# Performance work log

Hardware: AMD Instinct MI355X
Metric: run time of the kernel (lower is better)

## Reference

```python
import jax, jax.numpy as jnp
from jax import lax
import numpy as np

N = 64  # nPoints
N_ANGS = N * (N - 1) // 2

# lexicographic (top, btm) pair order used by OrthonormalMatrixGenerationSystem
_tops, _btms = np.triu_indices(N, k=1)
TOPS = jnp.asarray(_tops, dtype=jnp.int32)
BTMS = jnp.asarray(_btms, dtype=jnp.int32)


def build_R(angles, mus):
    """Sequential Givens-rotation chain: R = diag(mus) @ G_{nAngs-1} ... G_0 @ I."""
    def step(R, inp):
        ang, t, b = inp
        c, s = jnp.cos(ang), jnp.sin(ang)
        rt, rb = R[t], R[b]
        R = R.at[t].set(c * rt - s * rb).at[b].set(s * rt + c * rb)
        return R, None

    R0 = jnp.eye(N, dtype=angles.dtype)
    R, _ = lax.scan(step, R0, (angles, TOPS, BTMS))
    return mus[:, None] * R


def setup_inputs() -> dict:
    key = jax.random.key(0)
    k1, k2 = jax.random.split(key)
    X = jax.random.normal(k1, (N, 300000), dtype=jnp.float32)
    angles = jax.random.normal(k2, (N_ANGS,), dtype=jnp.float32)
    mus = jnp.ones((N,), dtype=jnp.float32)
    return {"X": X, "angles": angles, "mus": mus}


def reference(X, angles, mus):
    # mode='Analysis': Y = R @ X
    R = build_R(angles, mus)
    return R @ X
```

## Files before the change

### kernel.cpp

```cpp
#include <hip/hip_runtime.h>


#define NPTS  64
#define NANG  2016
#define NCOLS 300000
#define NC4   (NCOLS / 4)

typedef float v4 __attribute__((ext_vector_type(4)));

#define PSTR 68


__device__ __forceinline__ float rl(float x, int lane) {
    return __uint_as_float(__builtin_amdgcn_readlane(__float_as_uint(x), lane));
}

template<int T, int TB, int TA, int NG>
__device__ __forceinline__ void groups_run(float (&S)[NPTS],
                                           const float (&c)[NG], const float (&s)[NG],
                                           float* __restrict__ slab, int lane)
{
    if constexpr (T < TB) {
        constexpr int g   = T - TA;
        constexpr int LEN = 63 - T;
        float rt = S[0];
        #pragma unroll
        for (int i = 1; i <= LEN; ++i) {
            const float cc = rl(c[g], i - 1);
            const float ss = rl(s[g], i - 1);
            const float rb = S[i];
            S[i - 1] = fmaf(ss, rt, cc * rb);
            rt       = fmaf(cc, rt, -ss * rb);
        }
        slab[T * PSTR + lane] = rt;
        groups_run<T + 1, TB, TA, NG>(S, c, s, slab, lane);
    }
}

template<int TA, int TB>
__device__ __forceinline__ void do_wave(const float* __restrict__ angles,
                                        float* __restrict__ slab, int lane)
{
    constexpr int NG = TB - TA;
    float c[NG], s[NG];
    #pragma unroll
    for (int g = 0; g < NG; ++g) {
        const int t    = TA + g;
        const int base = 63 * t - (t * (t - 1)) / 2;
        float a = 0.0f;
        if (lane < 63 - t) a = angles[base + lane];
        sincosf(a, &s[g], &c[g]);
    }

    float S[NPTS];
    #pragma unroll
    for (int j = 0; j < NPTS; ++j) S[j] = (TA + j == lane) ? 1.0f : 0.0f;

    groups_run<TA, TB, TA, NG>(S, c, s, slab, lane);

    #pragma unroll
    for (int j = 0; j <= 63 - TB; ++j)
        slab[(TB + j) * PSTR + lane] = S[j];
}

template<int RS>
__device__ __forceinline__ void combine_step(float* __restrict__ P,
                                             const float* __restrict__ Ms,
                                             int tid)
{
    const int c4 = tid & 15;
    const int rg = tid >> 4;
    constexpr int NR   = 64 - RS;
    constexpr int NIT  = (NR + 15) / 16;
    constexpr int K4_0 = RS / 4;

    v4 acc[NIT];
    #pragma unroll
    for (int it = 0; it < NIT; ++it) acc[it] = (v4)0.0f;

    #pragma unroll 2
    for (int k4 = K4_0; k4 < 16; ++k4) {
        v4 pv[4];
        #pragma unroll
        for (int j = 0; j < 4; ++j)
            pv[j] = *(const v4*)(P + (4 * k4 + j) * PSTR + 4 * c4);
        #pragma unroll
        for (int it = 0; it < NIT; ++it) {
            const int r = RS + rg + 16 * it;
            if (r < 64) {
                const v4 mv = *(const v4*)(Ms + r * PSTR + 4 * k4);
                acc[it] += pv[0] * mv.x;
                acc[it] += pv[1] * mv.y;
                acc[it] += pv[2] * mv.z;
                acc[it] += pv[3] * mv.w;
            }
        }
    }
    __syncthreads();
    #pragma unroll
    for (int it = 0; it < NIT; ++it) {
        const int r = RS + rg + 16 * it;
        if (r < 64) *(v4*)(P + r * PSTR + 4 * c4) = acc[it];
    }
    __syncthreads();
}

__global__ __launch_bounds__(256, 1) void ortho_build_R(
    const float* __restrict__ angles, const float* __restrict__ mus,
    float* __restrict__ AT_out)
{
    __shared__ float P[NPTS * PSTR];
    __shared__ float M[3][NPTS * PSTR];

    const int tid  = threadIdx.x;
    const int lane = tid & 63;
    const int wv   = tid >> 6;

    if      (wv == 0) do_wave< 0,  9>(angles, P,    lane);
    else if (wv == 1) do_wave< 9, 19>(angles, M[0], lane);
    else if (wv == 2) do_wave<19, 32>(angles, M[1], lane);
    else              do_wave<32, 63>(angles, M[2], lane);
    __syncthreads();

    combine_step< 9>(P, M[0], tid);
    combine_step<19>(P, M[1], tid);
    combine_step<32>(P, M[2], tid);

    #pragma unroll
    for (int i = 0; i < 16; ++i) {
        const int idx = i * 256 + tid;
        const int r   = idx & 63;
        const int k   = idx >> 6;
        AT_out[k * NPTS + r] = mus[r] * P[r * PSTR + k];
    }
}

__device__ __forceinline__ void step16(v4 (&acc)[16], const float* __restrict__ Ak,
                                       const v4 xv)
{
    #pragma unroll
    for (int q = 0; q < 4; ++q) {
        const v4 a = *(const v4*)(Ak + 4 * q);
        acc[4 * q + 0] += xv * a.x;
        acc[4 * q + 1] += xv * a.y;
        acc[4 * q + 2] += xv * a.z;
        acc[4 * q + 3] += xv * a.w;
    }
}

__global__ __launch_bounds__(256) void ortho_apply(
    const float* __restrict__ X, const float* __restrict__ AT,
    float* __restrict__ Y)
{
    const int tc = threadIdx.x & 63;
    const int wv = threadIdx.x >> 6;
    const int tr = __builtin_amdgcn_readfirstlane(wv);
    const int r0 = tr * 16;

    const int j4 = blockIdx.x * 64 + tc;
    if (j4 >= NC4) return;

    const v4* xp = (const v4*)X + j4;

    v4 acc[16];
    #pragma unroll
    for (int i = 0; i < 16; ++i) acc[i] = (v4)0.0f;

    v4 xa[4], xb[4];
    #pragma unroll
    for (int q = 0; q < 4; ++q) xa[q] = xp[q * NC4];

    for (int k0 = 0; k0 < NPTS; k0 += 8) {
        #pragma unroll
        for (int q = 0; q < 4; ++q) xb[q] = xp[(k0 + 4 + q) * NC4];
        #pragma unroll
        for (int q = 0; q < 4; ++q) step16(acc, AT + (k0 + q) * NPTS + r0, xa[q]);
        #pragma unroll
        for (int q = 0; q < 4; ++q) xa[q] = xp[((k0 + 8 + q) & 63) * NC4];
        #pragma unroll
        for (int q = 0; q < 4; ++q) step16(acc, AT + (k0 + 4 + q) * NPTS + r0, xb[q]);
    }

    #pragma unroll
    for (int i = 0; i < 16; ++i) {
        v4* yp = (v4*)(Y + (size_t)(r0 + i) * NCOLS) + j4;
        __builtin_nontemporal_store(acc[i], yp);
    }
}

extern "C" void kernel_launch(void* const* d_in, const int* in_sizes, int n_in,
                              void* d_out, int out_size, void* d_ws, size_t ws_size,
                              hipStream_t stream) {
    const float* X      = (const float*)d_in[0];
    const float* angles = (const float*)d_in[1];
    const float* mus    = (const float*)d_in[2];
    float* Y  = (float*)d_out;
    float* AT = (float*)d_ws;

    ortho_build_R<<<1, 256, 0, stream>>>(angles, mus, AT);

    const int nblk = (NC4 + 63) / 64;
    ortho_apply<<<nblk, 256, 0, stream>>>(X, AT, Y);
}
```

Before: 193.6 us.

## Compute R@X with split-bf16 MFMA (3-pass hi/lo) instead of FP32 FMA

The build kernel now writes R as a pre-swizzled table of bf16 high and low parts laid out in MFMA operand order. The apply kernel splits each X value into bf16 hi/lo on the fly and runs three 16x16x32 bf16 MFMAs per tile (hi*hi, hi*lo, lo*hi) to approximate the FP32 product. This replaces the scalar FP32 FMA loop with matrix cores to cut compute cost on a memory-heavy GEMM. It lowers precision slightly by dropping the lo*lo term, and uses narrower per-lane 4-byte loads and stores over 16-column tiles, which may hurt coalescing.

```diff
diff --git a/kernel.cpp b/kernel.cpp
--- a/kernel.cpp
+++ b/kernel.cpp
@@ -4,9 +4,11 @@
 #define NPTS  64
 #define NANG  2016
 #define NCOLS 300000
-#define NC4   (NCOLS / 4)
+#define NTILE (NCOLS / 16)
 
 typedef float v4 __attribute__((ext_vector_type(4)));
+typedef __attribute__((ext_vector_type(4))) float f32x4;
+typedef __attribute__((ext_vector_type(8))) short short8;
 
 #define PSTR 68
 
@@ -49,7 +51,9 @@
         const int base = 63 * t - (t * (t - 1)) / 2;
         float a = 0.0f;
         if (lane < 63 - t) a = angles[base + lane];
-        sincosf(a, &s[g], &c[g]);
+        float sv, cv;
+        sincosf(a, &sv, &cv);
+        s[g] = sv; c[g] = cv;
     }
 
     float S[NPTS];
@@ -107,7 +111,7 @@
 
 __global__ __launch_bounds__(256, 1) void ortho_build_R(
     const float* __restrict__ angles, const float* __restrict__ mus,
-    float* __restrict__ AT_out)
+    unsigned short* __restrict__ tab)
 {
     __shared__ float P[NPTS * PSTR];
     __shared__ float M[3][NPTS * PSTR];
@@ -127,65 +131,80 @@
     combine_step<32>(P, M[2], tid);
 
     #pragma unroll
-    for (int i = 0; i < 16; ++i) {
-        const int idx = i * 256 + tid;
-        const int r   = idx & 63;
-        const int k   = idx >> 6;
-        AT_out[k * NPTS + r] = mus[r] * P[r * PSTR + k];
-    }
-}
-
-__device__ __forceinline__ void step16(v4 (&acc)[16], const float* __restrict__ Ak,
-                                       const v4 xv)
-{
-    #pragma unroll
-    for (int q = 0; q < 4; ++q) {
-        const v4 a = *(const v4*)(Ak + 4 * q);
-        acc[4 * q + 0] += xv * a.x;
-        acc[4 * q + 1] += xv * a.y;
-        acc[4 * q + 2] += xv * a.z;
-        acc[4 * q + 3] += xv * a.w;
+    for (int it = 0; it < 16; ++it) {
+        const int e  = it * 256 + tid;
+        const int j  = e & 7;
+        const int l  = (e >> 3) & 63;
+        const int ks = (e >> 9) & 1;
+        const int rt = (e >> 10) & 3;
+        const int row = 16 * rt + (l & 15);
+        const int k   = 32 * ks + 8 * (l >> 4) + j;
+        const float val = mus[row] * P[row * PSTR + k];
+        const unsigned u  = __float_as_uint(val);
+        const float    d  = val - __uint_as_float(u & 0xffff0000u);
+        tab[e]        = (unsigned short)(u >> 16);
+        tab[4096 + e] = (unsigned short)(__float_as_uint(d) >> 16);
     }
 }
 
 __global__ __launch_bounds__(256) void ortho_apply(
-    const float* __restrict__ X, const float* __restrict__ AT,
+    const float* __restrict__ X, const unsigned short* __restrict__ tab,
     float* __restrict__ Y)
 {
-    const int tc = threadIdx.x & 63;
-    const int wv = threadIdx.x >> 6;
-    const int tr = __builtin_amdgcn_readfirstlane(wv);
-    const int r0 = tr * 16;
-
-    const int j4 = blockIdx.x * 64 + tc;
-    if (j4 >= NC4) return;
-
-    const v4* xp = (const v4*)X + j4;
-
-    v4 acc[16];
-    #pragma unroll
-    for (int i = 0; i < 16; ++i) acc[i] = (v4)0.0f;
-
-    v4 xa[4], xb[4];
-    #pragma unroll
-    for (int q = 0; q < 4; ++q) xa[q] = xp[q * NC4];
-
-    for (int k0 = 0; k0 < NPTS; k0 += 8) {
-        #pragma unroll
-        for (int q = 0; q < 4; ++q) xb[q] = xp[(k0 + 4 + q) * NC4];
-        #pragma unroll
-        for (int q = 0; q < 4; ++q) step16(acc, AT + (k0 + q) * NPTS + r0, xa[q]);
-        #pragma unroll
-        for (int q = 0; q < 4; ++q) xa[q] = xp[((k0 + 8 + q) & 63) * NC4];
-        #pragma unroll
-        for (int q = 0; q < 4; ++q) step16(acc, AT + (k0 + 4 + q) * NPTS + r0, xb[q]);
-    }
-
-    #pragma unroll
-    for (int i = 0; i < 16; ++i) {
-        v4* yp = (v4*)(Y + (size_t)(r0 + i) * NCOLS) + j4;
-        __builtin_nontemporal_store(acc[i], yp);
-    }
+    const int l    = threadIdx.x & 63;
+    const int wv   = threadIdx.x >> 6;
+    const int tile = blockIdx.x * 4 + wv;
+    if (tile >= NTILE) return;
+    const int col = tile * 16 + (l & 15);
+    const int g   = l >> 4;
+
+    const short8* At = (const short8*)tab;
+    short8 a[2][4][2];
+    #pragma unroll
+    for (int sp = 0; sp < 2; ++sp)
+        #pragma unroll
+        for (int rt = 0; rt < 4; ++rt)
+            #pragma unroll
+            for (int ks = 0; ks < 2; ++ks)
+                a[sp][rt][ks] = At[((sp * 4 + rt) * 2 + ks) * 64 + l];
+
+    f32x4 acc[4];
+    #pragma unroll
+    for (int rt = 0; rt < 4; ++rt) acc[rt] = (f32x4)0.0f;
+
+    const float* px = X + (size_t)(8 * g) * NCOLS + col;
+
+    #pragma unroll
+    for (int ks = 0; ks < 2; ++ks) {
+        float xv[8];
+        #pragma unroll
+        for (int j = 0; j < 8; ++j)
+            xv[j] = px[(size_t)(32 * ks + j) * NCOLS];
+
+        short8 b1, b2;
+        #pragma unroll
+        for (int j = 0; j < 8; ++j) {
+            const unsigned u = __float_as_uint(xv[j]);
+            b1[j] = (short)(u >> 16);
+            const float d = xv[j] - __uint_as_float(u & 0xffff0000u);
+            b2[j] = (short)(__float_as_uint(d) >> 16);
+        }
+
+        #pragma unroll
+        for (int rt = 0; rt < 4; ++rt) {
+            acc[rt] = __builtin_amdgcn_mfma_f32_16x16x32_bf16(a[0][rt][ks], b1, acc[rt], 0, 0, 0);
+            acc[rt] = __builtin_amdgcn_mfma_f32_16x16x32_bf16(a[0][rt][ks], b2, acc[rt], 0, 0, 0);
+            acc[rt] = __builtin_amdgcn_mfma_f32_16x16x32_bf16(a[1][rt][ks], b1, acc[rt], 0, 0, 0);
+        }
+    }
+
+    #pragma unroll
+    for (int rt = 0; rt < 4; ++rt)
+        #pragma unroll
+        for (int r = 0; r < 4; ++r) {
+            const int row = 16 * rt + 4 * g + r;
+            __builtin_nontemporal_store(acc[rt][r], Y + (size_t)row * NCOLS + col);
+        }
 }
 
 extern "C" void kernel_launch(void* const* d_in, const int* in_sizes, int n_in,
@@ -194,11 +213,11 @@
     const float* X      = (const float*)d_in[0];
     const float* angles = (const float*)d_in[1];
     const float* mus    = (const float*)d_in[2];
-    float* Y  = (float*)d_out;
-    float* AT = (float*)d_ws;
-
-    ortho_build_R<<<1, 256, 0, stream>>>(angles, mus, AT);
-
-    const int nblk = (NC4 + 63) / 64;
-    ortho_apply<<<nblk, 256, 0, stream>>>(X, AT, Y);
-}
+    float* Y = (float*)d_out;
+    unsigned short* tab = (unsigned short*)d_ws;
+
+    ortho_build_R<<<1, 256, 0, stream>>>(angles, mus, tab);
+
+    const int nblk = (NTILE + 3) / 4;
+    ortho_apply<<<nblk, 256, 0, stream>>>(X, tab, Y);
+}
```

New measurement: 205.0 us. 1.06x slower.

## Split output rows across four blocks per column group in apply kernel

Applied to the files above, without the earlier changes.

The apply kernel now assigns each block one of four 16-row groups, so every thread computes only 4 output rows instead of 16. The grid grows fourfold and register pressure drops enough to request 8 blocks per SM through launch bounds, aiming at higher occupancy and better latency hiding. In exchange, each column of X is now read by four separate blocks, which raises global and L2 read traffic. The sincos temporaries change is cosmetic.

```diff
diff --git a/kernel.cpp b/kernel.cpp
--- a/kernel.cpp
+++ b/kernel.cpp
@@ -1,5 +1,4 @@
 #include <hip/hip_runtime.h>
-
 
 #define NPTS  64
 #define NANG  2016
@@ -49,7 +48,9 @@
         const int base = 63 * t - (t * (t - 1)) / 2;
         float a = 0.0f;
         if (lane < 63 - t) a = angles[base + lane];
-        sincosf(a, &s[g], &c[g]);
+        float sv, cv;
+        sincosf(a, &sv, &cv);
+        s[g] = sv; c[g] = cv;
     }
 
     float S[NPTS];
@@ -135,36 +136,25 @@
     }
 }
 
-__device__ __forceinline__ void step16(v4 (&acc)[16], const float* __restrict__ Ak,
-                                       const v4 xv)
-{
-    #pragma unroll
-    for (int q = 0; q < 4; ++q) {
-        const v4 a = *(const v4*)(Ak + 4 * q);
-        acc[4 * q + 0] += xv * a.x;
-        acc[4 * q + 1] += xv * a.y;
-        acc[4 * q + 2] += xv * a.z;
-        acc[4 * q + 3] += xv * a.w;
-    }
-}
-
-__global__ __launch_bounds__(256) void ortho_apply(
+__global__ __launch_bounds__(256, 8) void ortho_apply(
     const float* __restrict__ X, const float* __restrict__ AT,
     float* __restrict__ Y)
 {
     const int tc = threadIdx.x & 63;
     const int wv = threadIdx.x >> 6;
     const int tr = __builtin_amdgcn_readfirstlane(wv);
-    const int r0 = tr * 16;
-
-    const int j4 = blockIdx.x * 64 + tc;
+    const int rg = blockIdx.x & 3;
+    const int cg = blockIdx.x >> 2;
+    const int r0 = rg * 16 + tr * 4;
+
+    const int j4 = cg * 64 + tc;
     if (j4 >= NC4) return;
 
     const v4* xp = (const v4*)X + j4;
 
-    v4 acc[16];
-    #pragma unroll
-    for (int i = 0; i < 16; ++i) acc[i] = (v4)0.0f;
+    v4 acc[4];
+    #pragma unroll
+    for (int i = 0; i < 4; ++i) acc[i] = (v4)0.0f;
 
     v4 xa[4], xb[4];
     #pragma unroll
@@ -174,15 +164,27 @@
         #pragma unroll
         for (int q = 0; q < 4; ++q) xb[q] = xp[(k0 + 4 + q) * NC4];
         #pragma unroll
-        for (int q = 0; q < 4; ++q) step16(acc, AT + (k0 + q) * NPTS + r0, xa[q]);
+        for (int q = 0; q < 4; ++q) {
+            const v4 a = *(const v4*)(AT + (k0 + q) * NPTS + r0);
+            acc[0] += xa[q] * a.x;
+            acc[1] += xa[q] * a.y;
+            acc[2] += xa[q] * a.z;
+            acc[3] += xa[q] * a.w;
+        }
         #pragma unroll
         for (int q = 0; q < 4; ++q) xa[q] = xp[((k0 + 8 + q) & 63) * NC4];
         #pragma unroll
-        for (int q = 0; q < 4; ++q) step16(acc, AT + (k0 + 4 + q) * NPTS + r0, xb[q]);
-    }
-
-    #pragma unroll
-    for (int i = 0; i < 16; ++i) {
+        for (int q = 0; q < 4; ++q) {
+            const v4 a = *(const v4*)(AT + (k0 + 4 + q) * NPTS + r0);
+            acc[0] += xb[q] * a.x;
+            acc[1] += xb[q] * a.y;
+            acc[2] += xb[q] * a.z;
+            acc[3] += xb[q] * a.w;
+        }
+    }
+
+    #pragma unroll
+    for (int i = 0; i < 4; ++i) {
         v4* yp = (v4*)(Y + (size_t)(r0 + i) * NCOLS) + j4;
         __builtin_nontemporal_store(acc[i], yp);
     }
@@ -199,6 +201,6 @@
 
     ortho_build_R<<<1, 256, 0, stream>>>(angles, mus, AT);
 
-    const int nblk = (NC4 + 63) / 64;
+    const int nblk = ((NC4 + 63) / 64) * 4;
     ortho_apply<<<nblk, 256, 0, stream>>>(X, AT, Y);
 }
```

After: 229.7 us. 1.19x slower.

## Rebalance Givens build into uniform padded loops and split apply rows across eight waves

Applied to the files above, without the earlier changes.

The R-building kernel replaces per-wave templated, fully unrolled group chains with a runtime loop. Each wave takes 16 row groups (the last wave takes 15), padded to a fixed 63-step inner loop with identity rotations, and the next angle's sincos is computed one iteration ahead. The combine steps move to split points 16/32/48. The apply kernel goes from 256 to 512 threads per block, each wave computing 8 output rows instead of 16, which cuts accumulator registers to raise occupancy. The cost is twice as many X loads per block, mostly served from cache, and extra padded rotation work in the serial build.

```diff
diff --git a/kernel.cpp b/kernel.cpp
--- a/kernel.cpp
+++ b/kernel.cpp
@@ -1,5 +1,4 @@
 #include <hip/hip_runtime.h>
-
 
 #define NPTS  64
 #define NANG  2016
@@ -15,52 +14,21 @@
     return __uint_as_float(__builtin_amdgcn_readlane(__float_as_uint(x), lane));
 }
 
-template<int T, int TB, int TA, int NG>
-__device__ __forceinline__ void groups_run(float (&S)[NPTS],
-                                           const float (&c)[NG], const float (&s)[NG],
-                                           float* __restrict__ slab, int lane)
-{
-    if constexpr (T < TB) {
-        constexpr int g   = T - TA;
-        constexpr int LEN = 63 - T;
-        float rt = S[0];
-        #pragma unroll
-        for (int i = 1; i <= LEN; ++i) {
-            const float cc = rl(c[g], i - 1);
-            const float ss = rl(s[g], i - 1);
-            const float rb = S[i];
-            S[i - 1] = fmaf(ss, rt, cc * rb);
-            rt       = fmaf(cc, rt, -ss * rb);
-        }
-        slab[T * PSTR + lane] = rt;
-        groups_run<T + 1, TB, TA, NG>(S, c, s, slab, lane);
-    }
-}
-
-template<int TA, int TB>
-__device__ __forceinline__ void do_wave(const float* __restrict__ angles,
-                                        float* __restrict__ slab, int lane)
-{
-    constexpr int NG = TB - TA;
-    float c[NG], s[NG];
-    #pragma unroll
-    for (int g = 0; g < NG; ++g) {
-        const int t    = TA + g;
-        const int base = 63 * t - (t * (t - 1)) / 2;
-        float a = 0.0f;
-        if (lane < 63 - t) a = angles[base + lane];
-        sincosf(a, &s[g], &c[g]);
-    }
-
-    float S[NPTS];
-    #pragma unroll
-    for (int j = 0; j < NPTS; ++j) S[j] = (TA + j == lane) ? 1.0f : 0.0f;
-
-    groups_run<TA, TB, TA, NG>(S, c, s, slab, lane);
-
-    #pragma unroll
-    for (int j = 0; j <= 63 - TB; ++j)
-        slab[(TB + j) * PSTR + lane] = S[j];
+__device__ __forceinline__ float load_ang(const float* __restrict__ angles,
+                                          int t, int lane) {
+    int base = 63 * t - (t * (t - 1)) / 2;
+    int idx  = base + lane;
+    idx = idx < NANG ? idx : NANG - 1;
+    return angles[idx];
+}
+
+__device__ __forceinline__ void make_cs(float a, int t, int lane,
+                                        float& c, float& s) {
+    const int real = 63 - t;
+    const float ang = (lane < real) ? a : 0.0f;
+    float sv, cv;
+    sincosf(ang, &sv, &cv);
+    s = sv; c = cv;
 }
 
 template<int RS>
@@ -87,20 +55,18 @@
         #pragma unroll
         for (int it = 0; it < NIT; ++it) {
             const int r = RS + rg + 16 * it;
-            if (r < 64) {
-                const v4 mv = *(const v4*)(Ms + r * PSTR + 4 * k4);
-                acc[it] += pv[0] * mv.x;
-                acc[it] += pv[1] * mv.y;
-                acc[it] += pv[2] * mv.z;
-                acc[it] += pv[3] * mv.w;
-            }
+            const v4 mv = *(const v4*)(Ms + r * PSTR + 4 * k4);
+            acc[it] += pv[0] * mv.x;
+            acc[it] += pv[1] * mv.y;
+            acc[it] += pv[2] * mv.z;
+            acc[it] += pv[3] * mv.w;
         }
     }
     __syncthreads();
     #pragma unroll
     for (int it = 0; it < NIT; ++it) {
         const int r = RS + rg + 16 * it;
-        if (r < 64) *(v4*)(P + r * PSTR + 4 * c4) = acc[it];
+        *(v4*)(P + r * PSTR + 4 * c4) = acc[it];
     }
     __syncthreads();
 }
@@ -116,15 +82,58 @@
     const int lane = tid & 63;
     const int wv   = tid >> 6;
 
-    if      (wv == 0) do_wave< 0,  9>(angles, P,    lane);
-    else if (wv == 1) do_wave< 9, 19>(angles, M[0], lane);
-    else if (wv == 2) do_wave<19, 32>(angles, M[1], lane);
-    else              do_wave<32, 63>(angles, M[2], lane);
+    float* slab = (wv == 0) ? P : M[wv - 1];
+    const int TA = 16 * wv;
+    const int TB = (wv == 3) ? 63 : TA + 16;
+
+    float S[64];
+    #pragma unroll
+    for (int j = 0; j < 64; ++j) S[j] = (TA + j == lane) ? 1.0f : 0.0f;
+
+    float c0, s0;
+    {
+        const float a0 = load_ang(angles, TA, lane);
+        make_cs(a0, TA, lane, c0, s0);
+    }
+    float a1 = load_ang(angles, TA + 1, lane);
+
+    #pragma clang loop unroll(disable)
+    for (int t = TA; t < TB; ++t) {
+        const float a2 = load_ang(angles, t + 2, lane);
+        float c1, s1;
+        make_cs(a1, t + 1, lane, c1, s1);
+
+        float rt = S[0];
+        #pragma unroll
+        for (int i = 1; i <= 63; ++i) {
+            const float cc = rl(c0, i - 1);
+            const float ss = rl(s0, i - 1);
+            const float rb = S[i];
+            S[i - 1] = fmaf(ss, rt, cc * rb);
+            rt       = fmaf(cc, rt, -ss * rb);
+        }
+        slab[t * PSTR + lane] = rt;
+
+        c0 = c1; s0 = s1; a1 = a2;
+    }
+
+    if (wv == 0) {
+        #pragma unroll
+        for (int j = 0; j < 48; ++j) slab[(16 + j) * PSTR + lane] = S[j];
+    } else if (wv == 1) {
+        #pragma unroll
+        for (int j = 0; j < 32; ++j) slab[(32 + j) * PSTR + lane] = S[j];
+    } else if (wv == 2) {
+        #pragma unroll
+        for (int j = 0; j < 16; ++j) slab[(48 + j) * PSTR + lane] = S[j];
+    } else {
+        slab[63 * PSTR + lane] = S[0];
+    }
     __syncthreads();
 
-    combine_step< 9>(P, M[0], tid);
-    combine_step<19>(P, M[1], tid);
-    combine_step<32>(P, M[2], tid);
+    combine_step<16>(P, M[0], tid);
+    combine_step<32>(P, M[1], tid);
+    combine_step<48>(P, M[2], tid);
 
     #pragma unroll
     for (int i = 0; i < 16; ++i) {
@@ -135,36 +144,23 @@
     }
 }
 
-__device__ __forceinline__ void step16(v4 (&acc)[16], const float* __restrict__ Ak,
-                                       const v4 xv)
-{
-    #pragma unroll
-    for (int q = 0; q < 4; ++q) {
-        const v4 a = *(const v4*)(Ak + 4 * q);
-        acc[4 * q + 0] += xv * a.x;
-        acc[4 * q + 1] += xv * a.y;
-        acc[4 * q + 2] += xv * a.z;
-        acc[4 * q + 3] += xv * a.w;
-    }
-}
-
-__global__ __launch_bounds__(256) void ortho_apply(
+__global__ __launch_bounds__(512) void ortho_apply(
     const float* __restrict__ X, const float* __restrict__ AT,
     float* __restrict__ Y)
 {
     const int tc = threadIdx.x & 63;
     const int wv = threadIdx.x >> 6;
     const int tr = __builtin_amdgcn_readfirstlane(wv);
-    const int r0 = tr * 16;
+    const int r0 = tr * 8;
 
     const int j4 = blockIdx.x * 64 + tc;
     if (j4 >= NC4) return;
 
     const v4* xp = (const v4*)X + j4;
 
-    v4 acc[16];
-    #pragma unroll
-    for (int i = 0; i < 16; ++i) acc[i] = (v4)0.0f;
+    v4 acc[8];
+    #pragma unroll
+    for (int i = 0; i < 8; ++i) acc[i] = (v4)0.0f;
 
     v4 xa[4], xb[4];
     #pragma unroll
@@ -174,15 +170,29 @@
         #pragma unroll
         for (int q = 0; q < 4; ++q) xb[q] = xp[(k0 + 4 + q) * NC4];
         #pragma unroll
-        for (int q = 0; q < 4; ++q) step16(acc, AT + (k0 + q) * NPTS + r0, xa[q]);
+        for (int q = 0; q < 4; ++q) {
+            const v4 a  = *(const v4*)(AT + (k0 + q) * NPTS + r0);
+            const v4 a2 = *(const v4*)(AT + (k0 + q) * NPTS + r0 + 4);
+            acc[0] += xa[q] * a.x;  acc[1] += xa[q] * a.y;
+            acc[2] += xa[q] * a.z;  acc[3] += xa[q] * a.w;
+            acc[4] += xa[q] * a2.x; acc[5] += xa[q] * a2.y;
+            acc[6] += xa[q] * a2.z; acc[7] += xa[q] * a2.w;
+        }
         #pragma unroll
         for (int q = 0; q < 4; ++q) xa[q] = xp[((k0 + 8 + q) & 63) * NC4];
         #pragma unroll
-        for (int q = 0; q < 4; ++q) step16(acc, AT + (k0 + 4 + q) * NPTS + r0, xb[q]);
-    }
-
-    #pragma unroll
-    for (int i = 0; i < 16; ++i) {
+        for (int q = 0; q < 4; ++q) {
+            const v4 a  = *(const v4*)(AT + (k0 + 4 + q) * NPTS + r0);
+            const v4 a2 = *(const v4*)(AT + (k0 + 4 + q) * NPTS + r0 + 4);
+            acc[0] += xb[q] * a.x;  acc[1] += xb[q] * a.y;
+            acc[2] += xb[q] * a.z;  acc[3] += xb[q] * a.w;
+            acc[4] += xb[q] * a2.x; acc[5] += xb[q] * a2.y;
+            acc[6] += xb[q] * a2.z; acc[7] += xb[q] * a2.w;
+        }
+    }
+
+    #pragma unroll
+    for (int i = 0; i < 8; ++i) {
         v4* yp = (v4*)(Y + (size_t)(r0 + i) * NCOLS) + j4;
         __builtin_nontemporal_store(acc[i], yp);
     }
@@ -200,5 +210,5 @@
     ortho_build_R<<<1, 256, 0, stream>>>(angles, mus, AT);
 
     const int nblk = (NC4 + 63) / 64;
-    ortho_apply<<<nblk, 256, 0, stream>>>(X, AT, Y);
-}
+    ortho_apply<<<nblk, 512, 0, stream>>>(X, AT, Y);
+}
```

Result: faster. 176.2 us (-9.0%).
